# Kernel optimization log

Measured on AMD Instinct MI355X. Metric: run time of the kernel, lower is better.

## Reference

```python
import jax, jax.numpy as jnp
from jax import lax
import numpy as np

B, S, R, V, C = 64, 512, 64, 30522, 2


def setup_inputs() -> dict:
    key = jax.random.key(0)
    k1, k2, k3, k4 = jax.random.split(key, 4)
    input_ids = jax.random.randint(k1, (B, S), 0, V, dtype=jnp.int32)
    mask = jnp.ones((B, S), dtype=jnp.int32)
    segment_ids = jnp.zeros((B, S), dtype=jnp.int32)
    seq_lengths = jnp.full((B,), S, dtype=jnp.int32)
    # scale 1/sqrt(R) keeps the 512-step matrix chain numerically stable in fp32
    G_weight = jax.random.normal(k2, (V, R * R), dtype=jnp.float32) * (1.0 / float(np.sqrt(R)))
    G1_weight = jax.random.normal(k3, (R, 1), dtype=jnp.float32) * 0.1
    lin_W = jax.random.normal(k4, (C, R), dtype=jnp.float32) * 0.1
    lin_b = jnp.zeros((C,), dtype=jnp.float32)
    return {"input_ids": input_ids, "mask": mask, "segment_ids": segment_ids,
            "seq_lengths": seq_lengths, "G_weight": G_weight, "G1_weight": G1_weight,
            "lin_W": lin_W, "lin_b": lin_b}


def reference(input_ids, mask, segment_ids, seq_lengths, G_weight, G1_weight, lin_W, lin_b):
    b, s = input_ids.shape
    r = lin_W.shape[1]
    # embedding lookup -> per-token r x r matrices: (b, s, r, r)
    encoded = jnp.take(G_weight, input_ids, axis=0).reshape(b, s, r, r)
    # initial state: G1.weight.view(-1, r) repeated over batch -> (b, 1, r)
    init = jnp.broadcast_to(G1_weight.reshape(1, 1, r), (b, 1, r)).astype(G_weight.dtype)
    # sequential matrix-chain recurrence over sequence positions
    xs = jnp.moveaxis(encoded, 1, 0)  # (s, b, r, r)

    def step(carry, M):
        return jnp.einsum('bij,bjk->bik', carry, M), None

    result, _ = lax.scan(step, init, xs)  # (b, 1, r)
    # torch F.normalize(dim=2): x / max(||x||_2, eps)
    norm = jnp.sqrt(jnp.sum(result * result, axis=2, keepdims=True))
    normed = result / jnp.maximum(norm, 1e-12)
    encoded_x = jnp.squeeze(normed, axis=1)  # (b, r)
    out = encoded_x @ lin_W.T + lin_b  # (b, n_class)
    return jnp.squeeze(out)
```

## Files before the change

### kernel.cpp

```cpp
#include <hip/hip_runtime.h>
#include <math.h>

#define SEQ   512
#define RDIM  64
#define NB    64
#define SEGL  16
#define SEGS  32

typedef short  v4s __attribute__((ext_vector_type(4)));
typedef float  v4f __attribute__((ext_vector_type(4)));
typedef short  s8v __attribute__((ext_vector_type(8)));
typedef unsigned int u32x2 __attribute__((ext_vector_type(2)));

__device__ __forceinline__ v4f mfma16(v4s a, v4s b, v4f c) {
#if __has_builtin(__builtin_amdgcn_mfma_f32_16x16x16bf16_1k)
    return __builtin_amdgcn_mfma_f32_16x16x16bf16_1k(a, b, c, 0, 0, 0);
#else
    v4f d;
    asm volatile("v_mfma_f32_16x16x16_bf16 %0, %1, %2, %3"
                 : "=v"(d) : "v"(a), "v"(b), "v"(c));
    return d;
#endif
}

__device__ __forceinline__ unsigned short bf16_rne(float x) {
    unsigned int u = __float_as_uint(x);
    unsigned int r = u + 0x7FFFu + ((u >> 16) & 1u);
    return (unsigned short)(r >> 16);
}
__device__ __forceinline__ float bf16_tof(unsigned short h) {
    return __uint_as_float(((unsigned int)h) << 16);
}

__global__ __launch_bounds__(256, 3)
void seg_kernel(const int* __restrict__ input_ids,
                const float* __restrict__ G_weight,
                float* __restrict__ ws)
{
    __shared__ s8v bexch[2][16][64];

    const int tid = threadIdx.x;
    const int l   = tid & 63;
    const int w   = tid >> 6;
    const int g   = l >> 4;
    const int rl  = l & 15;
    const int blk = blockIdx.x;
    const int b   = blk >> 5;
    const int s   = blk & 31;

    int mseq[16];
#pragma unroll
    for (int i = 0; i < 16; ++i)
        mseq[i] = input_ids[(b << 9) + (s << 4) + (15 - i)];

    v4f acc[4];
    {
        const float* p0 = G_weight + (((size_t)__builtin_amdgcn_readfirstlane(mseq[0])) << 12);
#pragma unroll
        for (int jb = 0; jb < 4; ++jb)
#pragma unroll
            for (int r = 0; r < 4; ++r)
                acc[jb][r] = p0[(((w << 4) + (g << 2) + r) << 6) + (jb << 4) + rl];
    }

    const size_t aoff = (size_t)((((w << 4) + rl) << 6) + (g << 2));
    float4 pA0[4], pA1[4], pA2[4], pA3[4];

#define ISSUEA(P, IDX) do {                                                \
        const float* gp_ = G_weight + (((size_t)(IDX)) << 12) + aoff;      \
        P[0] = *(const float4*)(gp_);                                      \
        P[1] = *(const float4*)(gp_ + 16);                                 \
        P[2] = *(const float4*)(gp_ + 32);                                 \
        P[3] = *(const float4*)(gp_ + 48);                                 \
    } while (0)

    ISSUEA(pA0, __builtin_amdgcn_readfirstlane(mseq[1]));
    ISSUEA(pA1, __builtin_amdgcn_readfirstlane(mseq[2]));
    ISSUEA(pA2, __builtin_amdgcn_readfirstlane(mseq[3]));
    ISSUEA(pA3, __builtin_amdgcn_readfirstlane(mseq[4]));

#define SBODY(P, I) do {                                                        \
        const int pb_ = (I) & 1;                                                \
                                         \
        _Pragma("unroll")                                                       \
        for (int jb = 0; jb < 4; ++jb) {                                        \
            s8v pk;                                                             \
            _Pragma("unroll")                                                   \
            for (int r = 0; r < 4; ++r) {                                       \
                const unsigned short h_ = bf16_rne(acc[jb][r]);                 \
                pk[r]     = (short)h_;                                          \
                pk[4 + r] = (short)bf16_rne(acc[jb][r] - bf16_tof(h_));         \
            }                                                                   \
            bexch[pb_][(w << 2) + jb][l] = pk;                                  \
        }                                                                       \
                                                   \
        v4s Ah[4], Al[4];                                                       \
        _Pragma("unroll")                                                       \
        for (int kc = 0; kc < 4; ++kc) {                                        \
            const float e_[4] = {P[kc].x, P[kc].y, P[kc].z, P[kc].w};           \
            _Pragma("unroll")                                                   \
            for (int j = 0; j < 4; ++j) {                                       \
                const unsigned short h_ = bf16_rne(e_[j]);                      \
                Ah[kc][j] = (short)h_;                                          \
                Al[kc][j] = (short)bf16_rne(e_[j] - bf16_tof(h_));              \
            }                                                                   \
        }                                                                       \
        if ((I) + 4 <= 15)                                                      \
            ISSUEA(P, __builtin_amdgcn_readfirstlane(mseq[(I) + 4]));           \
        asm volatile("s_waitcnt lgkmcnt(0)\n\ts_barrier" ::: "memory");         \
        v4f na[4] = {{0,0,0,0},{0,0,0,0},{0,0,0,0},{0,0,0,0}};                  \
        _Pragma("unroll")                                                       \
        for (int kc = 0; kc < 4; ++kc) {                                        \
            _Pragma("unroll")                                                   \
            for (int jb = 0; jb < 4; ++jb) {                                    \
                const s8v q_ = bexch[pb_][(kc << 2) + jb][l];                   \
                const v4s qh = {q_[0], q_[1], q_[2], q_[3]};                    \
                const v4s ql = {q_[4], q_[5], q_[6], q_[7]};                    \
                na[jb] = mfma16(Ah[kc], qh, na[jb]);                            \
                na[jb] = mfma16(Al[kc], qh, na[jb]);                            \
                na[jb] = mfma16(Ah[kc], ql, na[jb]);                            \
            }                                                                   \
        }                                                                       \
        _Pragma("unroll")                                                       \
        for (int jb = 0; jb < 4; ++jb) acc[jb] = na[jb];                        \
    } while (0)

    SBODY(pA0,  1); SBODY(pA1,  2); SBODY(pA2,  3); SBODY(pA3,  4);
    SBODY(pA0,  5); SBODY(pA1,  6); SBODY(pA2,  7); SBODY(pA3,  8);
    SBODY(pA0,  9); SBODY(pA1, 10); SBODY(pA2, 11); SBODY(pA3, 12);
    SBODY(pA0, 13); SBODY(pA1, 14); SBODY(pA2, 15);

    float* wp = ws + (((size_t)blk) << 12);
#pragma unroll
    for (int jb = 0; jb < 4; ++jb)
#pragma unroll
        for (int r = 0; r < 4; ++r)
            wp[(((w << 4) + (g << 2) + r) << 6) + (jb << 4) + rl] = acc[jb][r];
}

__device__ __forceinline__ float qreduce4(float x) {
#if __has_builtin(__builtin_amdgcn_permlane16_swap) && __has_builtin(__builtin_amdgcn_permlane32_swap)
    u32x2 a = __builtin_amdgcn_permlane16_swap(__float_as_uint(x), __float_as_uint(x), false, false);
    const float y = __uint_as_float(a.x) + __uint_as_float(a.y);
    u32x2 c = __builtin_amdgcn_permlane32_swap(__float_as_uint(y), __float_as_uint(y), false, false);
    return __uint_as_float(c.x) + __uint_as_float(c.y);
#else
    x += __shfl_xor(x, 16, 64);
    x += __shfl_xor(x, 32, 64);
    return x;
#endif
}

#define STRD 12

__global__ __launch_bounds__(512, 2)
void chain2_kernel(const float* __restrict__ ws,
                   const float* __restrict__ G1_weight,
                   const float* __restrict__ lin_W,
                   const float* __restrict__ lin_b,
                   float* __restrict__ out)
{
    __shared__ __align__(16) float part[2][RDIM][STRD];

    const int tid  = threadIdx.x;
    const int lane = tid & 63;
    const int w    = tid >> 6;
    const int b    = blockIdx.x;
    const int sub  = lane >> 4;
    const int p16  = lane & 15;

    const int k0 = (w << 3) + sub;
    float vm0 = G1_weight[k0];
    float vm1 = G1_weight[k0 + 4];

    const size_t lo0 = (size_t)((w << 9) + (sub << 6) + (p16 << 2));
    const size_t lo1 = lo0 + 256;

    float4 bufA[16], bufB[16];

#define ISSUE2(S, T) do {                                                  \
        const float* bp_ = ws + (((size_t)((b << 5) + (T))) << 12);        \
        bufA[S] = *(const float4*)(bp_ + lo0);                             \
        bufB[S] = *(const float4*)(bp_ + lo1);                             \
    } while (0)

#pragma unroll
    for (int p = 0; p < 16; ++p) ISSUE2(p, p);

#define BODY2(S, T) do {                                                       \
        const float4 a_ = bufA[S];                                             \
        const float4 c_ = bufB[S];                                             \
        float fx = fmaf(vm0, a_.x, vm1 * c_.x);                                \
        float fy = fmaf(vm0, a_.y, vm1 * c_.y);                                \
        float fz = fmaf(vm0, a_.z, vm1 * c_.z);                                \
        float fw = fmaf(vm0, a_.w, vm1 * c_.w);                                \
        { int nx_ = (T) + 16; nx_ = (nx_ < SEGS) ? nx_ : (SEGS - 1);           \
          ISSUE2(S, nx_); }                                                    \
        fx = qreduce4(fx); fy = qreduce4(fy);                                  \
        fz = qreduce4(fz); fw = qreduce4(fw);                                  \
        const float wv_ = (sub == 0) ? fx : (sub == 1) ? fy                    \
                        : (sub == 2) ? fz : fw;                                \
        part[(T) & 1][(p16 << 2) + sub][w] = wv_;                              \
        asm volatile("s_waitcnt lgkmcnt(0)\n\ts_barrier" ::: "memory");        \
        {                                                                      \
            const float4* pk0_ = (const float4*)&part[(T) & 1][k0][0];         \
            const float4  r0_  = pk0_[0], r1_ = pk0_[1];                       \
            vm0 = ((r0_.x + r0_.y) + (r0_.z + r0_.w))                          \
                + ((r1_.x + r1_.y) + (r1_.z + r1_.w));                         \
            const float4* pk1_ = (const float4*)&part[(T) & 1][k0 + 4][0];     \
            const float4  s0_  = pk1_[0], s1_ = pk1_[1];                       \
            vm1 = ((s0_.x + s0_.y) + (s0_.z + s0_.w))                          \
                + ((s1_.x + s1_.y) + (s1_.z + s1_.w));                         \
        }                                                                      \
    } while (0)

    BODY2( 0,  0); BODY2( 1,  1); BODY2( 2,  2); BODY2( 3,  3);
    BODY2( 4,  4); BODY2( 5,  5); BODY2( 6,  6); BODY2( 7,  7);
    BODY2( 8,  8); BODY2( 9,  9); BODY2(10, 10); BODY2(11, 11);
    BODY2(12, 12); BODY2(13, 13); BODY2(14, 14); BODY2(15, 15);
    BODY2( 0, 16); BODY2( 1, 17); BODY2( 2, 18); BODY2( 3, 19);
    BODY2( 4, 20); BODY2( 5, 21); BODY2( 6, 22); BODY2( 7, 23);
    BODY2( 8, 24); BODY2( 9, 25); BODY2(10, 26); BODY2(11, 27);
    BODY2(12, 28); BODY2(13, 29); BODY2(14, 30); BODY2(15, 31);

    asm volatile("s_waitcnt vmcnt(0)" ::: "memory");

    float vj;
    {
        const float4* pj = (const float4*)&part[1][lane][0];
        const float4 q0 = pj[0], q1 = pj[1];
        vj = ((q0.x + q0.y) + (q0.z + q0.w)) + ((q1.x + q1.y) + (q1.z + q1.w));
    }

    if (w == 0) {
        float ss = vj * vj;
#pragma unroll
        for (int off = 32; off >= 1; off >>= 1)
            ss += __shfl_xor(ss, off, 64);
        const float inv = 1.0f / fmaxf(sqrtf(ss), 1e-12f);
        const float nj  = vj * inv;

        float d0 = nj * lin_W[lane];
        float d1 = nj * lin_W[RDIM + lane];
#pragma unroll
        for (int off = 32; off >= 1; off >>= 1) {
            d0 += __shfl_xor(d0, off, 64);
            d1 += __shfl_xor(d1, off, 64);
        }
        if (lane == 0) {
            out[b * 2 + 0] = d0 + lin_b[0];
            out[b * 2 + 1] = d1 + lin_b[1];
        }
    }
}

__global__ __launch_bounds__(512, 2)
void matchain_kernel(const int* __restrict__ input_ids,
                     const float* __restrict__ G_weight,
                     const float* __restrict__ G1_weight,
                     const float* __restrict__ lin_W,
                     const float* __restrict__ lin_b,
                     float* __restrict__ out)
{
    __shared__ int   ids[SEQ];
    __shared__ __align__(16) float part[2][RDIM][STRD];

    const int tid  = threadIdx.x;
    const int lane = tid & 63;
    const int w    = tid >> 6;
    const int b    = blockIdx.x;
    const int sub  = lane >> 4;
    const int p16  = lane & 15;

    ids[tid] = input_ids[b * SEQ + tid];
    __syncthreads();

    const int k0 = (w << 3) + sub;
    float vm0 = G1_weight[k0];
    float vm1 = G1_weight[k0 + 4];

    const size_t lo0 = (size_t)((w << 9) + (sub << 6) + (p16 << 2));
    const size_t lo1 = lo0 + 256;

    float4 bufA[16], bufB[16];

#define ISSUE(S, id_) do {                                        \
        const float* bp_ = G_weight + (((size_t)(id_)) << 12);    \
        bufA[S] = *(const float4*)(bp_ + lo0);                    \
        bufB[S] = *(const float4*)(bp_ + lo1);                    \
    } while (0)

#pragma unroll
    for (int p = 0; p < 16; ++p)
        ISSUE(p, __builtin_amdgcn_readfirstlane(ids[p]));

    int pend = ids[16];

#define BODY(S, K) do {                                                        \
        const float4 a_ = bufA[S];                                             \
        const float4 c_ = bufB[S];                                             \
        float fx = fmaf(vm0, a_.x, vm1 * c_.x);                                \
        float fy = fmaf(vm0, a_.y, vm1 * c_.y);                                \
        float fz = fmaf(vm0, a_.z, vm1 * c_.z);                                \
        float fw = fmaf(vm0, a_.w, vm1 * c_.w);                                \
        {                                                                      \
            const int idn_ = __builtin_amdgcn_readfirstlane(pend);             \
            ISSUE(S, idn_);                                                    \
            int nx_ = t0 + (K) + 17;                                           \
            nx_ = (nx_ < SEQ) ? nx_ : (SEQ - 1);                               \
            pend = ids[nx_];                                                   \
        }                                                                      \
        fx = qreduce4(fx); fy = qreduce4(fy);                                  \
        fz = qreduce4(fz); fw = qreduce4(fw);                                  \
        const float wv_ = (sub == 0) ? fx : (sub == 1) ? fy                    \
                        : (sub == 2) ? fz : fw;                                \
        part[(K) & 1][(p16 << 2) + sub][w] = wv_;                              \
        asm volatile("s_waitcnt lgkmcnt(0)\n\ts_barrier" ::: "memory");        \
        {                                                                      \
            const float4* pk0_ = (const float4*)&part[(K) & 1][k0][0];         \
            const float4  r0_  = pk0_[0], r1_ = pk0_[1];                       \
            vm0 = ((r0_.x + r0_.y) + (r0_.z + r0_.w))                          \
                + ((r1_.x + r1_.y) + (r1_.z + r1_.w));                         \
            const float4* pk1_ = (const float4*)&part[(K) & 1][k0 + 4][0];     \
            const float4  s0_  = pk1_[0], s1_ = pk1_[1];                       \
            vm1 = ((s0_.x + s0_.y) + (s0_.z + s0_.w))                          \
                + ((s1_.x + s1_.y) + (s1_.z + s1_.w));                         \
        }                                                                      \
    } while (0)

#pragma unroll 1
    for (int t0 = 0; t0 < SEQ; t0 += 16) {
        BODY( 0,  0); BODY( 1,  1); BODY( 2,  2); BODY( 3,  3);
        BODY( 4,  4); BODY( 5,  5); BODY( 6,  6); BODY( 7,  7);
        BODY( 8,  8); BODY( 9,  9); BODY(10, 10); BODY(11, 11);
        BODY(12, 12); BODY(13, 13); BODY(14, 14); BODY(15, 15);
    }

    asm volatile("s_waitcnt vmcnt(0)" ::: "memory");

    float vj;
    {
        const float4* pj = (const float4*)&part[1][lane][0];
        const float4 q0 = pj[0], q1 = pj[1];
        vj = ((q0.x + q0.y) + (q0.z + q0.w)) + ((q1.x + q1.y) + (q1.z + q1.w));
    }

    if (w == 0) {
        float ss = vj * vj;
#pragma unroll
        for (int off = 32; off >= 1; off >>= 1)
            ss += __shfl_xor(ss, off, 64);
        const float inv = 1.0f / fmaxf(sqrtf(ss), 1e-12f);
        const float nj  = vj * inv;

        float d0 = nj * lin_W[lane];
        float d1 = nj * lin_W[RDIM + lane];
#pragma unroll
        for (int off = 32; off >= 1; off >>= 1) {
            d0 += __shfl_xor(d0, off, 64);
            d1 += __shfl_xor(d1, off, 64);
        }
        if (lane == 0) {
            out[b * 2 + 0] = d0 + lin_b[0];
            out[b * 2 + 1] = d1 + lin_b[1];
        }
    }
}

extern "C" void kernel_launch(void* const* d_in, const int* in_sizes, int n_in,
                              void* d_out, int out_size, void* d_ws, size_t ws_size,
                              hipStream_t stream) {
    const int*   input_ids = (const int*)d_in[0];
    const float* G_weight  = (const float*)d_in[4];
    const float* G1_weight = (const float*)d_in[5];
    const float* lin_W     = (const float*)d_in[6];
    const float* lin_b     = (const float*)d_in[7];
    float*       out       = (float*)d_out;

    const size_t need = (size_t)NB * SEGS * RDIM * RDIM * sizeof(float);
    if (ws_size >= need) {
        float* ws = (float*)d_ws;
        seg_kernel<<<NB * SEGS, 256, 0, stream>>>(input_ids, G_weight, ws);
        chain2_kernel<<<NB, 512, 0, stream>>>(ws, G1_weight, lin_W, lin_b, out);
    } else {
        matchain_kernel<<<NB, 512, 0, stream>>>(input_ids, G_weight, G1_weight,
                                                lin_W, lin_b, out);
    }
}
```

Baseline: 121.3 us.

## Compute each segment product in a single wavefront without LDS exchange

Restructures seg_kernel so one 64-lane wavefront computes the whole 64x64 segment product. The accumulator is held in registers as 4x4 MFMA tiles, which removes the LDS B-matrix exchange and the per-step block barrier. The chain now starts from the identity, so 16 multiplies run instead of 15, and each step prefetches only the next token's matrix, one step ahead. The trade-off is a large register footprint (64-float accumulators plus 16 float4 prefetches), lower occupancy, and a shallower prefetch, so load latency may be exposed.

```diff
diff --git a/kernel.cpp b/kernel.cpp
--- a/kernel.cpp
+++ b/kernel.cpp
@@ -9,7 +9,6 @@
 
 typedef short  v4s __attribute__((ext_vector_type(4)));
 typedef float  v4f __attribute__((ext_vector_type(4)));
-typedef short  s8v __attribute__((ext_vector_type(8)));
 typedef unsigned int u32x2 __attribute__((ext_vector_type(2)));
 
 __device__ __forceinline__ v4f mfma16(v4s a, v4s b, v4f c) {
@@ -32,110 +31,111 @@
     return __uint_as_float(((unsigned int)h) << 16);
 }
 
-__global__ __launch_bounds__(256, 3)
+__global__ __launch_bounds__(64, 2)
 void seg_kernel(const int* __restrict__ input_ids,
                 const float* __restrict__ G_weight,
                 float* __restrict__ ws)
 {
-    __shared__ s8v bexch[2][16][64];
-
-    const int tid = threadIdx.x;
-    const int l   = tid & 63;
-    const int w   = tid >> 6;
-    const int g   = l >> 4;
-    const int rl  = l & 15;
-    const int blk = blockIdx.x;
-    const int b   = blk >> 5;
-    const int s   = blk & 31;
-
-    int mseq[16];
-#pragma unroll
-    for (int i = 0; i < 16; ++i)
-        mseq[i] = input_ids[(b << 9) + (s << 4) + (15 - i)];
-
-    v4f acc[4];
+    const int lane = threadIdx.x & 63;
+    const int g    = lane >> 4;
+    const int rl   = lane & 15;
+    const int blk  = blockIdx.x;
+    const int idb  = blk << 4;
+
+    v4f acc[4][4];
+#pragma unroll
+    for (int m = 0; m < 4; ++m)
+#pragma unroll
+        for (int jb = 0; jb < 4; ++jb)
+#pragma unroll
+            for (int r = 0; r < 4; ++r)
+                acc[m][jb][r] = (m == jb && rl == ((g << 2) + r)) ? 1.0f : 0.0f;
+
+    float4 pa[16];
     {
-        const float* p0 = G_weight + (((size_t)__builtin_amdgcn_readfirstlane(mseq[0])) << 12);
+        const int id0 = __builtin_amdgcn_readfirstlane(input_ids[idb + 15]);
+        const float* bp = G_weight + (((size_t)id0) << 12);
+#pragma unroll
+        for (int m = 0; m < 4; ++m) {
+            const float* gp = bp + (((m << 4) + rl) << 6) + (g << 2);
+#pragma unroll
+            for (int kc = 0; kc < 4; ++kc)
+                pa[(m << 2) + kc] = *(const float4*)(gp + (kc << 4));
+        }
+    }
+
+    int pend = input_ids[idb + 14];
+
+#pragma unroll 1
+    for (int i = 0; i < 16; ++i) {
+        v4s Bh[4][4], Bl[4][4];
+#pragma unroll
+        for (int kc = 0; kc < 4; ++kc)
+#pragma unroll
+            for (int jb = 0; jb < 4; ++jb) {
+                v4s h, l;
+#pragma unroll
+                for (int r = 0; r < 4; ++r) {
+                    const float x = acc[kc][jb][r];
+                    const unsigned short hh = bf16_rne(x);
+                    h[r] = (short)hh;
+                    l[r] = (short)bf16_rne(x - bf16_tof(hh));
+                }
+                Bh[kc][jb] = h;
+                Bl[kc][jb] = l;
+            }
+
+        const int idn = __builtin_amdgcn_readfirstlane(pend);
+
+#pragma unroll
+        for (int m = 0; m < 4; ++m) {
+            v4s Ah[4], Al[4];
+#pragma unroll
+            for (int kc = 0; kc < 4; ++kc) {
+                const float4 x = pa[(m << 2) + kc];
+                const float e[4] = {x.x, x.y, x.z, x.w};
+#pragma unroll
+                for (int j = 0; j < 4; ++j) {
+                    const unsigned short hh = bf16_rne(e[j]);
+                    Ah[kc][j] = (short)hh;
+                    Al[kc][j] = (short)bf16_rne(e[j] - bf16_tof(hh));
+                }
+            }
+            if (i < 15) {
+                const float* gp = G_weight + (((size_t)idn) << 12)
+                                + (((m << 4) + rl) << 6) + (g << 2);
+#pragma unroll
+                for (int kc = 0; kc < 4; ++kc)
+                    pa[(m << 2) + kc] = *(const float4*)(gp + (kc << 4));
+            }
+#pragma unroll
+            for (int jb = 0; jb < 4; ++jb) {
+                v4f d = {0.f, 0.f, 0.f, 0.f};
+#pragma unroll
+                for (int kc = 0; kc < 4; ++kc) {
+                    d = mfma16(Ah[kc], Bh[kc][jb], d);
+                    d = mfma16(Al[kc], Bh[kc][jb], d);
+                    d = mfma16(Ah[kc], Bl[kc][jb], d);
+                }
+                acc[m][jb] = d;
+            }
+        }
+
+        {
+            int nx = 13 - i;
+            nx = (nx < 0) ? 0 : nx;
+            pend = input_ids[idb + nx];
+        }
+    }
+
+    float* wp = ws + (((size_t)blk) << 12);
+#pragma unroll
+    for (int m = 0; m < 4; ++m)
 #pragma unroll
         for (int jb = 0; jb < 4; ++jb)
 #pragma unroll
             for (int r = 0; r < 4; ++r)
-                acc[jb][r] = p0[(((w << 4) + (g << 2) + r) << 6) + (jb << 4) + rl];
-    }
-
-    const size_t aoff = (size_t)((((w << 4) + rl) << 6) + (g << 2));
-    float4 pA0[4], pA1[4], pA2[4], pA3[4];
-
-#define ISSUEA(P, IDX) do {                                                \
-        const float* gp_ = G_weight + (((size_t)(IDX)) << 12) + aoff;      \
-        P[0] = *(const float4*)(gp_);                                      \
-        P[1] = *(const float4*)(gp_ + 16);                                 \
-        P[2] = *(const float4*)(gp_ + 32);                                 \
-        P[3] = *(const float4*)(gp_ + 48);                                 \
-    } while (0)
-
-    ISSUEA(pA0, __builtin_amdgcn_readfirstlane(mseq[1]));
-    ISSUEA(pA1, __builtin_amdgcn_readfirstlane(mseq[2]));
-    ISSUEA(pA2, __builtin_amdgcn_readfirstlane(mseq[3]));
-    ISSUEA(pA3, __builtin_amdgcn_readfirstlane(mseq[4]));
-
-#define SBODY(P, I) do {                                                        \
-        const int pb_ = (I) & 1;                                                \
-                                         \
-        _Pragma("unroll")                                                       \
-        for (int jb = 0; jb < 4; ++jb) {                                        \
-            s8v pk;                                                             \
-            _Pragma("unroll")                                                   \
-            for (int r = 0; r < 4; ++r) {                                       \
-                const unsigned short h_ = bf16_rne(acc[jb][r]);                 \
-                pk[r]     = (short)h_;                                          \
-                pk[4 + r] = (short)bf16_rne(acc[jb][r] - bf16_tof(h_));         \
-            }                                                                   \
-            bexch[pb_][(w << 2) + jb][l] = pk;                                  \
-        }                                                                       \
-                                                   \
-        v4s Ah[4], Al[4];                                                       \
-        _Pragma("unroll")                                                       \
-        for (int kc = 0; kc < 4; ++kc) {                                        \
-            const float e_[4] = {P[kc].x, P[kc].y, P[kc].z, P[kc].w};           \
-            _Pragma("unroll")                                                   \
-            for (int j = 0; j < 4; ++j) {                                       \
-                const unsigned short h_ = bf16_rne(e_[j]);                      \
-                Ah[kc][j] = (short)h_;                                          \
-                Al[kc][j] = (short)bf16_rne(e_[j] - bf16_tof(h_));              \
-            }                                                                   \
-        }                                                                       \
-        if ((I) + 4 <= 15)                                                      \
-            ISSUEA(P, __builtin_amdgcn_readfirstlane(mseq[(I) + 4]));           \
-        asm volatile("s_waitcnt lgkmcnt(0)\n\ts_barrier" ::: "memory");         \
-        v4f na[4] = {{0,0,0,0},{0,0,0,0},{0,0,0,0},{0,0,0,0}};                  \
-        _Pragma("unroll")                                                       \
-        for (int kc = 0; kc < 4; ++kc) {                                        \
-            _Pragma("unroll")                                                   \
-            for (int jb = 0; jb < 4; ++jb) {                                    \
-                const s8v q_ = bexch[pb_][(kc << 2) + jb][l];                   \
-                const v4s qh = {q_[0], q_[1], q_[2], q_[3]};                    \
-                const v4s ql = {q_[4], q_[5], q_[6], q_[7]};                    \
-                na[jb] = mfma16(Ah[kc], qh, na[jb]);                            \
-                na[jb] = mfma16(Al[kc], qh, na[jb]);                            \
-                na[jb] = mfma16(Ah[kc], ql, na[jb]);                            \
-            }                                                                   \
-        }                                                                       \
-        _Pragma("unroll")                                                       \
-        for (int jb = 0; jb < 4; ++jb) acc[jb] = na[jb];                        \
-    } while (0)
-
-    SBODY(pA0,  1); SBODY(pA1,  2); SBODY(pA2,  3); SBODY(pA3,  4);
-    SBODY(pA0,  5); SBODY(pA1,  6); SBODY(pA2,  7); SBODY(pA3,  8);
-    SBODY(pA0,  9); SBODY(pA1, 10); SBODY(pA2, 11); SBODY(pA3, 12);
-    SBODY(pA0, 13); SBODY(pA1, 14); SBODY(pA2, 15);
-
-    float* wp = ws + (((size_t)blk) << 12);
-#pragma unroll
-    for (int jb = 0; jb < 4; ++jb)
-#pragma unroll
-        for (int r = 0; r < 4; ++r)
-            wp[(((w << 4) + (g << 2) + r) << 6) + (jb << 4) + rl] = acc[jb][r];
+                wp[(((m << 4) + (g << 2) + r) << 6) + (jb << 4) + rl] = acc[m][jb][r];
 }
 
 __device__ __forceinline__ float qreduce4(float x) {
@@ -380,7 +380,7 @@
     const size_t need = (size_t)NB * SEGS * RDIM * RDIM * sizeof(float);
     if (ws_size >= need) {
         float* ws = (float*)d_ws;
-        seg_kernel<<<NB * SEGS, 256, 0, stream>>>(input_ids, G_weight, ws);
+        seg_kernel<<<NB * SEGS, 64, 0, stream>>>(input_ids, G_weight, ws);
         chain2_kernel<<<NB, 512, 0, stream>>>(ws, G1_weight, lin_W, lin_b, out);
     } else {
         matchain_kernel<<<NB, 512, 0, stream>>>(input_ids, G_weight, G1_weight,
```

Measured after the change: 125.0 us. 1.03x slower.
